# Performance work log

Hardware: AMD Instinct MI355X
Metric: run time of the kernel (lower is better)

## Reference

```python
import jax, jax.numpy as jnp
import numpy as np

FRAME_N = 8
CE_CODE_N = 8
UPSAMPLE = FRAME_N // CE_CODE_N
N_CAM = 2
C = 3
H, W = 720, 1280
B = 4
SIGMA_RANGE = (0.0, 1e-09)


def setup_inputs() -> dict:
    key = jax.random.key(0)
    k1, k2 = jax.random.split(key)
    frames = jax.random.normal(k1, (B, FRAME_N, C, H, W), dtype=jnp.float32)
    # nn.init.uniform_(ce_weight, a=-1, b=1)
    ce_weight = jax.random.uniform(k2, (CE_CODE_N, C, H, W, N_CAM), dtype=jnp.float32,
                                   minval=-1.0, maxval=1.0)
    return {"frames": frames, "ce_weight": ce_weight}


def _ste(x):
    # straight-through binarization (forward part only)
    return (x > 0).astype(x.dtype)


def reference(frames, ce_weight):
    ce_code = _ste(ce_weight)                       # (N, C, H, W, K) in {0,1}
    frames = frames[..., :H, :W]                    # (B, F, C, H, W)
    # temporal upsample: each code entry repeated UPSAMPLE times along frame axis
    ce_code_up = jnp.repeat(ce_code, UPSAMPLE, axis=0)          # (F, C, H, W, K)
    ce_code_up_ = jnp.broadcast_to(ce_code_up, (B,) + ce_code_up.shape)  # (B,F,C,H,W,K)

    # weighted sum over frames for each camera; complement uses sum(frames) - weighted
    weighted = jnp.einsum('bfchw,fchwk->bkchw', frames, ce_code_up) / FRAME_N  # (B,K,C,H,W)
    total = jnp.sum(frames, axis=1) / FRAME_N                                   # (B,C,H,W)
    comp = total[:, None] - weighted                                            # (B,K,C,H,W)

    # interleave [coded, complement] per camera -> channels 2*K*C
    ce_blur_img = jnp.stack([weighted, comp], axis=2).reshape(B, 2 * N_CAM * C, H, W)

    nk = jax.random.key(123)
    nk1, nk2 = jax.random.split(nk)
    noise_level = jax.random.uniform(nk1, (), dtype=jnp.float32,
                                     minval=SIGMA_RANGE[0], maxval=SIGMA_RANGE[1])
    ce_blur_img_noisy = ce_blur_img + noise_level * jax.random.normal(
        nk2, ce_blur_img.shape, dtype=jnp.float32)
    return ce_blur_img_noisy, ce_code_up_, ce_blur_img
```

## Files before the change

kernel.cpp:

```cpp
#include <hip/hip_runtime.h>

#define Fn 8
#define Bn 4
#define Kn 2

constexpr unsigned HW   = 720u * 1280u;
constexpr unsigned CHW  = 3u * HW;
constexpr unsigned OUT0 = Bn * 12u * HW;
constexpr unsigned OUT1 = (unsigned)Bn * Fn * CHW * Kn;

typedef float f4 __attribute__((ext_vector_type(4)));

__device__ __forceinline__ float stepf(float x) { return x > 0.0f ? 1.0f : 0.0f; }

__global__ __launch_bounds__(256) void cep_enc_kernel(const float* __restrict__ frames,
                                                      const float* __restrict__ cw,
                                                      float* __restrict__ out) {
    const unsigned q   = blockIdx.x * 256u + threadIdx.x;
    const unsigned chw = q * 4u;
    if (chw >= CHW) return;
    const unsigned c  = chw / HW;
    const unsigned hw = chw - c * HW;

    f4 ci[Fn][2];
#pragma unroll
    for (int f = 0; f < Fn; ++f) {
        const f4* p = reinterpret_cast<const f4*>(cw + (unsigned)f * (CHW * Kn) + chw * Kn);
        f4 a = p[0];
        f4 b = p[1];
        f4 sa, sb;
        sa.x = stepf(a.x); sa.y = stepf(a.y); sa.z = stepf(a.z); sa.w = stepf(a.w);
        sb.x = stepf(b.x); sb.y = stepf(b.y); sb.z = stepf(b.z); sb.w = stepf(b.w);
        ci[f][0] = sa;
        ci[f][1] = sb;
    }

    float* out0 = out;
    float* out1 = out + OUT0;
    float* out2 = out + OUT0 + OUT1;

    f4 fr[Fn];
#pragma unroll
    for (int f = 0; f < Fn; ++f)
        fr[f] = *reinterpret_cast<const f4*>(frames + (unsigned)f * CHW + chw);

#pragma unroll
    for (int b = 0; b < Bn; ++b) {
#pragma unroll
        for (int f = 0; f < Fn; ++f) {
            f4* p = reinterpret_cast<f4*>(out1 + (unsigned)(b * Fn + f) * (CHW * Kn) + chw * Kn);
            p[0] = ci[f][0];
            p[1] = ci[f][1];
        }
    }

    const float inv = 1.0f / (float)Fn;
#pragma unroll
    for (int b = 0; b < Bn; ++b) {
        float sx = 0.f, sy = 0.f, sz = 0.f, sw = 0.f;
        float ax = 0.f, ay = 0.f, az = 0.f, aw = 0.f;
        float bx = 0.f, by = 0.f, bz = 0.f, bw = 0.f;
        f4 cur[Fn];
#pragma unroll
        for (int f = 0; f < Fn; ++f) cur[f] = fr[f];

        if (b + 1 < Bn) {
#pragma unroll
            for (int f = 0; f < Fn; ++f)
                fr[f] = *reinterpret_cast<const f4*>(frames + (unsigned)((b + 1) * Fn + f) * CHW + chw);
        }

#pragma unroll
        for (int f = 0; f < Fn; ++f) {
            f4 v = cur[f];
            sx += v.x; sy += v.y; sz += v.z; sw += v.w;
            ax += v.x * ci[f][0].x;  ay += v.y * ci[f][0].z;
            az += v.z * ci[f][1].x;  aw += v.w * ci[f][1].z;
            bx += v.x * ci[f][0].y;  by += v.y * ci[f][0].w;
            bz += v.z * ci[f][1].y;  bw += v.w * ci[f][1].w;
        }
        sx *= inv; sy *= inv; sz *= inv; sw *= inv;
        ax *= inv; ay *= inv; az *= inv; aw *= inv;
        bx *= inv; by *= inv; bz *= inv; bw *= inv;

        f4 wk0 = {ax, ay, az, aw};
        f4 wk1 = {bx, by, bz, bw};
        f4 ck0 = {sx - ax, sy - ay, sz - az, sw - aw};
        f4 ck1 = {sx - bx, sy - by, sz - bz, sw - bw};

        const unsigned base = (unsigned)b * 12u * HW + hw;
        *reinterpret_cast<f4*>(out0 + base + (0u + c) * HW) = wk0;
        *reinterpret_cast<f4*>(out0 + base + (3u + c) * HW) = ck0;
        *reinterpret_cast<f4*>(out0 + base + (6u + c) * HW) = wk1;
        *reinterpret_cast<f4*>(out0 + base + (9u + c) * HW) = ck1;

        *reinterpret_cast<f4*>(out2 + base + (0u + c) * HW) = wk0;
        *reinterpret_cast<f4*>(out2 + base + (3u + c) * HW) = ck0;
        *reinterpret_cast<f4*>(out2 + base + (6u + c) * HW) = wk1;
        *reinterpret_cast<f4*>(out2 + base + (9u + c) * HW) = ck1;
    }
}

extern "C" void kernel_launch(void* const* d_in, const int* in_sizes, int n_in,
                              void* d_out, int out_size, void* d_ws, size_t ws_size,
                              hipStream_t stream) {
    const float* frames = (const float*)d_in[0];
    const float* cw     = (const float*)d_in[1];
    float* out          = (float*)d_out;

    constexpr unsigned quads = CHW / 4u;
    constexpr unsigned block = 256u;
    constexpr unsigned grid  = (quads + block - 1u) / block;
    cep_enc_kernel<<<grid, block, 0, stream>>>(frames, cw, out);
}
```

Measured before the change: 379.4 us.

## Split batches across waves and pack binary codes into bitmasks

Each block now maps its four waves to the four batch entries for the same 64 quads, instead of one thread looping over all batches. The binarized codes are held as two 32-bit bitmasks rather than 64 float registers, and launch bounds request higher occupancy. This is meant to cut register pressure and expose more memory-level parallelism. In exchange, each wave re-reads the ce_weight data for its quads, relying on cache to absorb the redundant loads.

```diff
diff --git a/kernel.cpp b/kernel.cpp
--- a/kernel.cpp
+++ b/kernel.cpp
@@ -11,94 +11,84 @@
 
 typedef float f4 __attribute__((ext_vector_type(4)));
 
-__device__ __forceinline__ float stepf(float x) { return x > 0.0f ? 1.0f : 0.0f; }
+__global__ __launch_bounds__(256, 8) void cep_enc_kernel(const float* __restrict__ frames,
+                                                         const float* __restrict__ cw,
+                                                         float* __restrict__ out) {
+    const unsigned lane = threadIdx.x & 63u;
+    const unsigned b    = threadIdx.x >> 6u;
+    const unsigned quad = blockIdx.x * 64u + lane;
+    const unsigned chw  = quad * 4u;
+    const unsigned c    = chw / HW;
+    const unsigned hw   = chw - c * HW;
 
-__global__ __launch_bounds__(256) void cep_enc_kernel(const float* __restrict__ frames,
-                                                      const float* __restrict__ cw,
-                                                      float* __restrict__ out) {
-    const unsigned q   = blockIdx.x * 256u + threadIdx.x;
-    const unsigned chw = q * 4u;
-    if (chw >= CHW) return;
-    const unsigned c  = chw / HW;
-    const unsigned hw = chw - c * HW;
-
-    f4 ci[Fn][2];
+    unsigned mk0 = 0u, mk1 = 0u;
 #pragma unroll
     for (int f = 0; f < Fn; ++f) {
         const f4* p = reinterpret_cast<const f4*>(cw + (unsigned)f * (CHW * Kn) + chw * Kn);
         f4 a = p[0];
-        f4 b = p[1];
-        f4 sa, sb;
-        sa.x = stepf(a.x); sa.y = stepf(a.y); sa.z = stepf(a.z); sa.w = stepf(a.w);
-        sb.x = stepf(b.x); sb.y = stepf(b.y); sb.z = stepf(b.z); sb.w = stepf(b.w);
-        ci[f][0] = sa;
-        ci[f][1] = sb;
+        f4 d = p[1];
+        mk0 |= (a.x > 0.f ? 1u : 0u) << (f * 4 + 0);
+        mk0 |= (a.z > 0.f ? 1u : 0u) << (f * 4 + 1);
+        mk0 |= (d.x > 0.f ? 1u : 0u) << (f * 4 + 2);
+        mk0 |= (d.z > 0.f ? 1u : 0u) << (f * 4 + 3);
+        mk1 |= (a.y > 0.f ? 1u : 0u) << (f * 4 + 0);
+        mk1 |= (a.w > 0.f ? 1u : 0u) << (f * 4 + 1);
+        mk1 |= (d.y > 0.f ? 1u : 0u) << (f * 4 + 2);
+        mk1 |= (d.w > 0.f ? 1u : 0u) << (f * 4 + 3);
     }
 
     float* out0 = out;
     float* out1 = out + OUT0;
     float* out2 = out + OUT0 + OUT1;
 
-    f4 fr[Fn];
-#pragma unroll
-    for (int f = 0; f < Fn; ++f)
-        fr[f] = *reinterpret_cast<const f4*>(frames + (unsigned)f * CHW + chw);
+    float sx = 0.f, sy = 0.f, sz = 0.f, sw = 0.f;
+    float ax = 0.f, ay = 0.f, az = 0.f, aw = 0.f;
+    float bx = 0.f, by = 0.f, bz = 0.f, bw = 0.f;
 
 #pragma unroll
-    for (int b = 0; b < Bn; ++b) {
-#pragma unroll
-        for (int f = 0; f < Fn; ++f) {
-            f4* p = reinterpret_cast<f4*>(out1 + (unsigned)(b * Fn + f) * (CHW * Kn) + chw * Kn);
-            p[0] = ci[f][0];
-            p[1] = ci[f][1];
-        }
+    for (int f = 0; f < Fn; ++f) {
+        f4 v = *reinterpret_cast<const f4*>(frames + (unsigned)(b * Fn + f) * CHW + chw);
+
+        const float c00 = (mk0 >> (f * 4 + 0)) & 1u ? 1.0f : 0.0f;
+        const float c01 = (mk0 >> (f * 4 + 1)) & 1u ? 1.0f : 0.0f;
+        const float c02 = (mk0 >> (f * 4 + 2)) & 1u ? 1.0f : 0.0f;
+        const float c03 = (mk0 >> (f * 4 + 3)) & 1u ? 1.0f : 0.0f;
+        const float c10 = (mk1 >> (f * 4 + 0)) & 1u ? 1.0f : 0.0f;
+        const float c11 = (mk1 >> (f * 4 + 1)) & 1u ? 1.0f : 0.0f;
+        const float c12 = (mk1 >> (f * 4 + 2)) & 1u ? 1.0f : 0.0f;
+        const float c13 = (mk1 >> (f * 4 + 3)) & 1u ? 1.0f : 0.0f;
+
+        f4 e0 = {c00, c10, c01, c11};
+        f4 e1 = {c02, c12, c03, c13};
+        f4* p = reinterpret_cast<f4*>(out1 + (unsigned)(b * Fn + f) * (CHW * Kn) + chw * Kn);
+        p[0] = e0;
+        p[1] = e1;
+
+        sx += v.x; sy += v.y; sz += v.z; sw += v.w;
+        ax += v.x * c00;  ay += v.y * c01;  az += v.z * c02;  aw += v.w * c03;
+        bx += v.x * c10;  by += v.y * c11;  bz += v.z * c12;  bw += v.w * c13;
     }
 
     const float inv = 1.0f / (float)Fn;
-#pragma unroll
-    for (int b = 0; b < Bn; ++b) {
-        float sx = 0.f, sy = 0.f, sz = 0.f, sw = 0.f;
-        float ax = 0.f, ay = 0.f, az = 0.f, aw = 0.f;
-        float bx = 0.f, by = 0.f, bz = 0.f, bw = 0.f;
-        f4 cur[Fn];
-#pragma unroll
-        for (int f = 0; f < Fn; ++f) cur[f] = fr[f];
+    sx *= inv; sy *= inv; sz *= inv; sw *= inv;
+    ax *= inv; ay *= inv; az *= inv; aw *= inv;
+    bx *= inv; by *= inv; bz *= inv; bw *= inv;
 
-        if (b + 1 < Bn) {
-#pragma unroll
-            for (int f = 0; f < Fn; ++f)
-                fr[f] = *reinterpret_cast<const f4*>(frames + (unsigned)((b + 1) * Fn + f) * CHW + chw);
-        }
+    f4 wk0 = {ax, ay, az, aw};
+    f4 wk1 = {bx, by, bz, bw};
+    f4 ck0 = {sx - ax, sy - ay, sz - az, sw - aw};
+    f4 ck1 = {sx - bx, sy - by, sz - bz, sw - bw};
 
-#pragma unroll
-        for (int f = 0; f < Fn; ++f) {
-            f4 v = cur[f];
-            sx += v.x; sy += v.y; sz += v.z; sw += v.w;
-            ax += v.x * ci[f][0].x;  ay += v.y * ci[f][0].z;
-            az += v.z * ci[f][1].x;  aw += v.w * ci[f][1].z;
-            bx += v.x * ci[f][0].y;  by += v.y * ci[f][0].w;
-            bz += v.z * ci[f][1].y;  bw += v.w * ci[f][1].w;
-        }
-        sx *= inv; sy *= inv; sz *= inv; sw *= inv;
-        ax *= inv; ay *= inv; az *= inv; aw *= inv;
-        bx *= inv; by *= inv; bz *= inv; bw *= inv;
+    const unsigned base = b * 12u * HW + hw;
+    *reinterpret_cast<f4*>(out0 + base + (0u + c) * HW) = wk0;
+    *reinterpret_cast<f4*>(out0 + base + (3u + c) * HW) = ck0;
+    *reinterpret_cast<f4*>(out0 + base + (6u + c) * HW) = wk1;
+    *reinterpret_cast<f4*>(out0 + base + (9u + c) * HW) = ck1;
 
-        f4 wk0 = {ax, ay, az, aw};
-        f4 wk1 = {bx, by, bz, bw};
-        f4 ck0 = {sx - ax, sy - ay, sz - az, sw - aw};
-        f4 ck1 = {sx - bx, sy - by, sz - bz, sw - bw};
-
-        const unsigned base = (unsigned)b * 12u * HW + hw;
-        *reinterpret_cast<f4*>(out0 + base + (0u + c) * HW) = wk0;
-        *reinterpret_cast<f4*>(out0 + base + (3u + c) * HW) = ck0;
-        *reinterpret_cast<f4*>(out0 + base + (6u + c) * HW) = wk1;
-        *reinterpret_cast<f4*>(out0 + base + (9u + c) * HW) = ck1;
-
-        *reinterpret_cast<f4*>(out2 + base + (0u + c) * HW) = wk0;
-        *reinterpret_cast<f4*>(out2 + base + (3u + c) * HW) = ck0;
-        *reinterpret_cast<f4*>(out2 + base + (6u + c) * HW) = wk1;
-        *reinterpret_cast<f4*>(out2 + base + (9u + c) * HW) = ck1;
-    }
+    *reinterpret_cast<f4*>(out2 + base + (0u + c) * HW) = wk0;
+    *reinterpret_cast<f4*>(out2 + base + (3u + c) * HW) = ck0;
+    *reinterpret_cast<f4*>(out2 + base + (6u + c) * HW) = wk1;
+    *reinterpret_cast<f4*>(out2 + base + (9u + c) * HW) = ck1;
 }
 
 extern "C" void kernel_launch(void* const* d_in, const int* in_sizes, int n_in,
@@ -109,7 +99,6 @@
     float* out          = (float*)d_out;
 
     constexpr unsigned quads = CHW / 4u;
-    constexpr unsigned block = 256u;
-    constexpr unsigned grid  = (quads + block - 1u) / block;
-    cep_enc_kernel<<<grid, block, 0, stream>>>(frames, cw, out);
+    constexpr unsigned grid  = quads / 64u;
+    cep_enc_kernel<<<grid, 256, 0, stream>>>(frames, cw, out);
 }
```

Result: slower. 496.6 us (+30.9%).

## Split into code-broadcast kernel and batch-parallel blur kernel with packed bitmask

Applied to the files above, without the earlier changes.

Splits the single fused kernel into two. The first binarizes the code weights, writes the broadcast code output and packs the binary code into a byte mask in workspace. The second computes the blurred images, with one grid dimension per batch, reading the compact mask instead of the float weights. The aim is more parallelism and fewer live registers per thread. In exchange it adds a second launch and a workspace round-trip of the mask, plus a fallback path when workspace is too small.

```diff
diff --git a/kernel.cpp b/kernel.cpp
--- a/kernel.cpp
+++ b/kernel.cpp
@@ -2,77 +2,146 @@
 
 #define Fn 8
 #define Bn 4
-#define Kn 2
 
-constexpr unsigned HW   = 720u * 1280u;
-constexpr unsigned CHW  = 3u * HW;
-constexpr unsigned OUT0 = Bn * 12u * HW;
-constexpr unsigned OUT1 = (unsigned)Bn * Fn * CHW * Kn;
+constexpr unsigned HW    = 720u * 1280u;
+constexpr unsigned CHW   = 3u * HW;
+constexpr unsigned QUADS = CHW / 4u;
+constexpr unsigned OUT0  = Bn * 12u * HW;
+constexpr unsigned OUT1  = (unsigned)Bn * Fn * CHW * 2u;
 
 typedef float f4 __attribute__((ext_vector_type(4)));
 
-__device__ __forceinline__ float stepf(float x) { return x > 0.0f ? 1.0f : 0.0f; }
+template<bool WRITE_MASK>
+__global__ __launch_bounds__(256) void bcast_kernel(const float* __restrict__ cw,
+                                                    float* __restrict__ out1,
+                                                    unsigned char* __restrict__ mask) {
+    const unsigned quad = blockIdx.x * 256u + threadIdx.x;
+    const unsigned f    = blockIdx.y;
 
-__global__ __launch_bounds__(256) void cep_enc_kernel(const float* __restrict__ frames,
+    const float* p = cw + (size_t)f * (CHW * 2u) + (size_t)quad * 8u;
+    const f4 a = *reinterpret_cast<const f4*>(p);
+    const f4 d = *reinterpret_cast<const f4*>(p + 4);
+
+    f4 sa, sd;
+    sa.x = a.x > 0.f ? 1.f : 0.f;  sa.y = a.y > 0.f ? 1.f : 0.f;
+    sa.z = a.z > 0.f ? 1.f : 0.f;  sa.w = a.w > 0.f ? 1.f : 0.f;
+    sd.x = d.x > 0.f ? 1.f : 0.f;  sd.y = d.y > 0.f ? 1.f : 0.f;
+    sd.z = d.z > 0.f ? 1.f : 0.f;  sd.w = d.w > 0.f ? 1.f : 0.f;
+
+#pragma unroll
+    for (int b = 0; b < Bn; ++b) {
+        f4* q = reinterpret_cast<f4*>(out1 + (size_t)(b * Fn + f) * (CHW * 2u) + (size_t)quad * 8u);
+        q[0] = sa;
+        q[1] = sd;
+    }
+
+    if (WRITE_MASK) {
+        unsigned m = (a.x > 0.f ? 1u : 0u)
+                   | (a.z > 0.f ? 2u : 0u)
+                   | (d.x > 0.f ? 4u : 0u)
+                   | (d.z > 0.f ? 8u : 0u)
+                   | (a.y > 0.f ? 16u : 0u)
+                   | (a.w > 0.f ? 32u : 0u)
+                   | (d.y > 0.f ? 64u : 0u)
+                   | (d.w > 0.f ? 128u : 0u);
+        mask[(size_t)f * QUADS + quad] = (unsigned char)m;
+    }
+}
+
+__global__ __launch_bounds__(256) void blur_mask_kernel(const float* __restrict__ frames,
+                                                        const unsigned char* __restrict__ mask,
+                                                        float* __restrict__ out) {
+    const unsigned quad = blockIdx.x * 256u + threadIdx.x;
+    const unsigned b    = blockIdx.y;
+    const unsigned chw  = quad * 4u;
+    const unsigned c    = chw / HW;
+    const unsigned hw   = chw - c * HW;
+
+    unsigned m[Fn];
+    f4 v[Fn];
+#pragma unroll
+    for (int f = 0; f < Fn; ++f) {
+        m[f] = mask[(size_t)f * QUADS + quad];
+        v[f] = *reinterpret_cast<const f4*>(frames + (size_t)(b * Fn + f) * CHW + chw);
+    }
+
+    float sx = 0.f, sy = 0.f, sz = 0.f, sw = 0.f;
+    float ax = 0.f, ay = 0.f, az = 0.f, aw = 0.f;
+    float bx = 0.f, by = 0.f, bz = 0.f, bw = 0.f;
+#pragma unroll
+    for (int f = 0; f < Fn; ++f) {
+        const float c00 = (m[f] & 1u)   ? 1.f : 0.f;
+        const float c01 = (m[f] & 2u)   ? 1.f : 0.f;
+        const float c02 = (m[f] & 4u)   ? 1.f : 0.f;
+        const float c03 = (m[f] & 8u)   ? 1.f : 0.f;
+        const float c10 = (m[f] & 16u)  ? 1.f : 0.f;
+        const float c11 = (m[f] & 32u)  ? 1.f : 0.f;
+        const float c12 = (m[f] & 64u)  ? 1.f : 0.f;
+        const float c13 = (m[f] & 128u) ? 1.f : 0.f;
+        sx += v[f].x; sy += v[f].y; sz += v[f].z; sw += v[f].w;
+        ax += v[f].x * c00;  ay += v[f].y * c01;  az += v[f].z * c02;  aw += v[f].w * c03;
+        bx += v[f].x * c10;  by += v[f].y * c11;  bz += v[f].z * c12;  bw += v[f].w * c13;
+    }
+
+    const float inv = 1.0f / (float)Fn;
+    sx *= inv; sy *= inv; sz *= inv; sw *= inv;
+    ax *= inv; ay *= inv; az *= inv; aw *= inv;
+    bx *= inv; by *= inv; bz *= inv; bw *= inv;
+
+    f4 wk0 = {ax, ay, az, aw};
+    f4 wk1 = {bx, by, bz, bw};
+    f4 ck0 = {sx - ax, sy - ay, sz - az, sw - aw};
+    f4 ck1 = {sx - bx, sy - by, sz - bz, sw - bw};
+
+    float* out0 = out;
+    float* out2 = out + OUT0 + OUT1;
+
+    const unsigned base = b * 12u * HW + hw;
+    *reinterpret_cast<f4*>(out0 + base + (0u + c) * HW) = wk0;
+    *reinterpret_cast<f4*>(out0 + base + (3u + c) * HW) = ck0;
+    *reinterpret_cast<f4*>(out0 + base + (6u + c) * HW) = wk1;
+    *reinterpret_cast<f4*>(out0 + base + (9u + c) * HW) = ck1;
+
+    *reinterpret_cast<f4*>(out2 + base + (0u + c) * HW) = wk0;
+    *reinterpret_cast<f4*>(out2 + base + (3u + c) * HW) = ck0;
+    *reinterpret_cast<f4*>(out2 + base + (6u + c) * HW) = wk1;
+    *reinterpret_cast<f4*>(out2 + base + (9u + c) * HW) = ck1;
+}
+
+__global__ __launch_bounds__(256) void blur_cw_kernel(const float* __restrict__ frames,
                                                       const float* __restrict__ cw,
                                                       float* __restrict__ out) {
-    const unsigned q   = blockIdx.x * 256u + threadIdx.x;
-    const unsigned chw = q * 4u;
-    if (chw >= CHW) return;
-    const unsigned c  = chw / HW;
-    const unsigned hw = chw - c * HW;
+    const unsigned quad = blockIdx.x * 256u + threadIdx.x;
+    const unsigned chw  = quad * 4u;
+    const unsigned c    = chw / HW;
+    const unsigned hw   = chw - c * HW;
 
     f4 ci[Fn][2];
 #pragma unroll
     for (int f = 0; f < Fn; ++f) {
-        const f4* p = reinterpret_cast<const f4*>(cw + (unsigned)f * (CHW * Kn) + chw * Kn);
-        f4 a = p[0];
-        f4 b = p[1];
-        f4 sa, sb;
-        sa.x = stepf(a.x); sa.y = stepf(a.y); sa.z = stepf(a.z); sa.w = stepf(a.w);
-        sb.x = stepf(b.x); sb.y = stepf(b.y); sb.z = stepf(b.z); sb.w = stepf(b.w);
+        const f4* p = reinterpret_cast<const f4*>(cw + (size_t)f * (CHW * 2u) + (size_t)quad * 8u);
+        f4 a = p[0], d = p[1];
+        f4 sa, sd;
+        sa.x = a.x > 0.f ? 1.f : 0.f;  sa.y = a.y > 0.f ? 1.f : 0.f;
+        sa.z = a.z > 0.f ? 1.f : 0.f;  sa.w = a.w > 0.f ? 1.f : 0.f;
+        sd.x = d.x > 0.f ? 1.f : 0.f;  sd.y = d.y > 0.f ? 1.f : 0.f;
+        sd.z = d.z > 0.f ? 1.f : 0.f;  sd.w = d.w > 0.f ? 1.f : 0.f;
         ci[f][0] = sa;
-        ci[f][1] = sb;
+        ci[f][1] = sd;
     }
 
     float* out0 = out;
-    float* out1 = out + OUT0;
     float* out2 = out + OUT0 + OUT1;
+    const float inv = 1.0f / (float)Fn;
 
-    f4 fr[Fn];
-#pragma unroll
-    for (int f = 0; f < Fn; ++f)
-        fr[f] = *reinterpret_cast<const f4*>(frames + (unsigned)f * CHW + chw);
-
-#pragma unroll
-    for (int b = 0; b < Bn; ++b) {
-#pragma unroll
-        for (int f = 0; f < Fn; ++f) {
-            f4* p = reinterpret_cast<f4*>(out1 + (unsigned)(b * Fn + f) * (CHW * Kn) + chw * Kn);
-            p[0] = ci[f][0];
-            p[1] = ci[f][1];
-        }
-    }
-
-    const float inv = 1.0f / (float)Fn;
 #pragma unroll
     for (int b = 0; b < Bn; ++b) {
         float sx = 0.f, sy = 0.f, sz = 0.f, sw = 0.f;
         float ax = 0.f, ay = 0.f, az = 0.f, aw = 0.f;
         float bx = 0.f, by = 0.f, bz = 0.f, bw = 0.f;
-        f4 cur[Fn];
-#pragma unroll
-        for (int f = 0; f < Fn; ++f) cur[f] = fr[f];
-
-        if (b + 1 < Bn) {
-#pragma unroll
-            for (int f = 0; f < Fn; ++f)
-                fr[f] = *reinterpret_cast<const f4*>(frames + (unsigned)((b + 1) * Fn + f) * CHW + chw);
-        }
-
 #pragma unroll
         for (int f = 0; f < Fn; ++f) {
-            f4 v = cur[f];
+            f4 v = *reinterpret_cast<const f4*>(frames + (size_t)(b * Fn + f) * CHW + chw);
             sx += v.x; sy += v.y; sz += v.z; sw += v.w;
             ax += v.x * ci[f][0].x;  ay += v.y * ci[f][0].z;
             az += v.z * ci[f][1].x;  aw += v.w * ci[f][1].z;
@@ -88,12 +157,11 @@
         f4 ck0 = {sx - ax, sy - ay, sz - az, sw - aw};
         f4 ck1 = {sx - bx, sy - by, sz - bz, sw - bw};
 
-        const unsigned base = (unsigned)b * 12u * HW + hw;
+        const unsigned base = b * 12u * HW + hw;
         *reinterpret_cast<f4*>(out0 + base + (0u + c) * HW) = wk0;
         *reinterpret_cast<f4*>(out0 + base + (3u + c) * HW) = ck0;
         *reinterpret_cast<f4*>(out0 + base + (6u + c) * HW) = wk1;
         *reinterpret_cast<f4*>(out0 + base + (9u + c) * HW) = ck1;
-
         *reinterpret_cast<f4*>(out2 + base + (0u + c) * HW) = wk0;
         *reinterpret_cast<f4*>(out2 + base + (3u + c) * HW) = ck0;
         *reinterpret_cast<f4*>(out2 + base + (6u + c) * HW) = wk1;
@@ -107,9 +175,16 @@
     const float* frames = (const float*)d_in[0];
     const float* cw     = (const float*)d_in[1];
     float* out          = (float*)d_out;
+    unsigned char* mask = (unsigned char*)d_ws;
 
-    constexpr unsigned quads = CHW / 4u;
-    constexpr unsigned block = 256u;
-    constexpr unsigned grid  = (quads + block - 1u) / block;
-    cep_enc_kernel<<<grid, block, 0, stream>>>(frames, cw, out);
+    constexpr unsigned xblocks = QUADS / 256u;
+    const bool use_mask = ws_size >= (size_t)QUADS * Fn;
+
+    if (use_mask) {
+        bcast_kernel<true><<<dim3(xblocks, Fn), 256, 0, stream>>>(cw, out + OUT0, mask);
+        blur_mask_kernel<<<dim3(xblocks, Bn), 256, 0, stream>>>(frames, mask, out);
+    } else {
+        bcast_kernel<false><<<dim3(xblocks, Fn), 256, 0, stream>>>(cw, out + OUT0, mask);
+        blur_cw_kernel<<<xblocks, 256, 0, stream>>>(frames, cw, out);
+    }
 }
```

Result: faster. 314.2 us, median of 2 (-17.2%).
